# Optimization experiments

Measured on AMD Instinct MI355X. Metric: run time of the kernel, lower is better.

Reference implementation:

```python
import jax, jax.numpy as jnp
import numpy as np

N_NODES = 100000


def gcn_layer(x, W, b, src, dst, n):
    # PyG GCNConv: add self-loops, symmetric degree normalization,
    # message = norm * (x @ W)[src], aggregated (sum) at dst, plus bias.
    loops = jnp.arange(n, dtype=src.dtype)
    s = jnp.concatenate([src, loops])  # [E+N]
    d = jnp.concatenate([dst, loops])  # [E+N]
    deg = jnp.zeros((n,), x.dtype).at[d].add(jnp.ones((s.shape[0],), x.dtype))
    dinv = jnp.where(deg > 0, jax.lax.rsqrt(deg), 0.0)
    norm = dinv[s] * dinv[d]  # [E+N]
    h = x @ W  # [N, out]
    msg = h[s] * norm[:, None]  # [E+N, out]
    out = jax.ops.segment_sum(msg, d, num_segments=n)
    return out + b


def setup_inputs() -> dict:
    key = jax.random.key(0)
    k1, k2, k3, k4 = jax.random.split(key, 4)
    in_dim, hid_dim, out_dim = 128, 128, 64
    x = jax.random.normal(k1, (N_NODES, in_dim), dtype=jnp.float32)
    edge_index = jax.random.randint(k2, (2, 1600000), 0, N_NODES, dtype=jnp.int64)
    W1 = jax.random.normal(k3, (in_dim, hid_dim), dtype=jnp.float32) / np.sqrt(in_dim)
    b1 = jnp.zeros((hid_dim,), jnp.float32)
    W2 = jax.random.normal(k4, (hid_dim, out_dim), dtype=jnp.float32) / np.sqrt(hid_dim)
    b2 = jnp.zeros((out_dim,), jnp.float32)
    return {"x": x, "edge_index": edge_index, "W1": W1, "b1": b1, "W2": W2, "b2": b2}


def reference(x, edge_index, W1, b1, W2, b2):
    src, dst = edge_index[0], edge_index[1]
    h = gcn_layer(x, W1, b1, src, dst, N_NODES)
    h = jax.nn.relu(h)
    # F.dropout(training=False) -> identity (eval mode reference)
    out = gcn_layer(h, W2, b2, src, dst, N_NODES)
    return out
```

## Files before the change

kernel.cpp:

```cpp
#include <hip/hip_runtime.h>
#include <hip/hip_fp16.h>

#define NN 100000
#define NSB 256
#define WPS2 391
#define CAP2 8192
#define EPB 16

typedef _Float16 f16;
typedef _Float16 f16x8 __attribute__((ext_vector_type(8)));
typedef float f32x4 __attribute__((ext_vector_type(4)));

__device__ __forceinline__ int eload(const void* e, long i, int is64) {
  if (is64) return (int)((const long long*)e)[i];
  return ((const int*)e)[i];
}

__global__ __launch_bounds__(1024) void k_detect(const unsigned* __restrict__ e,
                                                 int* __restrict__ flag,
                                                 int* __restrict__ bcur2) {
  __shared__ unsigned red[1024];
  int t = threadIdx.x;
  if (t < NSB) bcur2[t] = t * CAP2;
  unsigned acc = e[1 + 2 * t] | e[1 + 2 * t + 2048];
  red[t] = acc;
  __syncthreads();
  for (int off = 512; off > 0; off >>= 1) {
    if (t < off) red[t] |= red[t + off];
    __syncthreads();
  }
  if (t == 0) *flag = (red[0] == 0) ? 1 : 0;
}

__global__ void k_wprep(const float* __restrict__ W1, const float* __restrict__ W2,
                        f16* __restrict__ Wt1, f16* __restrict__ Wt2) {
  int idx = blockIdx.x * 256 + threadIdx.x;
  if (idx < 128 * 128) {
    int k = idx / 128, n = idx % 128;
    Wt1[n * 128 + k] = (f16)W1[idx];
  } else {
    int i2 = idx - 128 * 128;
    if (i2 < 128 * 64) {
      int k = i2 / 64, n = i2 % 64;
      Wt2[n * 128 + k] = (f16)W2[i2];
    }
  }
}

__global__ __launch_bounds__(256) void k_split(const void* __restrict__ e,
                                               const int* __restrict__ flag,
                                               int E, int* __restrict__ bcur2,
                                               int* __restrict__ srcb,
                                               int* __restrict__ dstb) {
  __shared__ int hist[NSB];
  const int tid = threadIdx.x;
  const long b0 = (long)blockIdx.x * (256 * EPB);
  const int is64 = *flag;
  hist[tid] = 0;
  __syncthreads();

  int sv[EPB], dv[EPB];
#pragma unroll
  for (int j = 0; j < EPB; ++j) {
    long idx = b0 + j * 256 + tid;
    int s = 0, d = -1;
    if (idx < E) {
      s = eload(e, idx, is64);
      d = eload(e, (long)E + idx, is64);
    }
    sv[j] = s; dv[j] = d;
    if (d >= 0) atomicAdd(&hist[(unsigned)d / WPS2], 1);
  }
  __syncthreads();
  {
    int c = hist[tid];
    int base = (c > 0) ? atomicAdd(&bcur2[tid], c) : 0;
    __syncthreads();
    hist[tid] = base;
  }
  __syncthreads();
#pragma unroll
  for (int j = 0; j < EPB; ++j) {
    int d = dv[j];
    if (d < 0) continue;
    int pos = atomicAdd(&hist[(unsigned)d / WPS2], 1);
    srcb[pos] = sv[j];
    dstb[pos] = d;
  }
}

__global__ __launch_bounds__(256) void k_wscan(const int* __restrict__ bcur2,
                                               int* __restrict__ wbase,
                                               int* __restrict__ rowptr, int E) {
  __shared__ int sm[NSB];
  int t = threadIdx.x;
  int c = bcur2[t] - t * CAP2;
  sm[t] = c;
  __syncthreads();
  for (int off = 1; off < NSB; off <<= 1) {
    int a = (t >= off) ? sm[t - off] : 0;
    __syncthreads();
    sm[t] += a;
    __syncthreads();
  }
  wbase[t] = sm[t] - c;
  if (t == 0) rowptr[NN] = E;
}

__global__ __launch_bounds__(256) void k_build(const int* __restrict__ dstb,
                                               const int* __restrict__ srcb,
                                               const int* __restrict__ bcur2,
                                               const int* __restrict__ wbase,
                                               int* __restrict__ rowptr,
                                               float* __restrict__ dinv,
                                               int* __restrict__ csr) {
  __shared__ int lc[512];
  __shared__ int cur[512];
  const int tid = threadIdx.x;
  const int b = blockIdx.x;
  const int nlo = b * WPS2;
  const int nhi = (nlo + WPS2 < NN) ? nlo + WPS2 : NN;
  const int nw = nhi - nlo;
  lc[tid] = 0; lc[tid + 256] = 0;
  __syncthreads();
  const int cnt = bcur2[b] - b * CAP2;
  const long s0 = (long)b * CAP2;
  for (int i = tid; i < cnt; i += 256)
    atomicAdd(&lc[dstb[s0 + i] - nlo], 1);
  __syncthreads();
  for (int off = 1; off < 512; off <<= 1) {
    int a0 = (tid >= off) ? lc[tid - off] : 0;
    int a1 = (tid + 256 >= off) ? lc[tid + 256 - off] : 0;
    __syncthreads();
    lc[tid] += a0; lc[tid + 256] += a1;
    __syncthreads();
  }
  const int wb = wbase[b];
#pragma unroll
  for (int h = 0; h < 2; ++h) {
    int j = tid + h * 256;
    if (j < nw) {
      int inc = lc[j];
      int c = inc - (j > 0 ? lc[j - 1] : 0);
      int ex = wb + inc - c;
      rowptr[nlo + j] = ex;
      dinv[nlo + j] = rsqrtf((float)c + 1.0f);
      cur[j] = ex;
    }
  }
  __syncthreads();
  for (int i = tid; i < cnt; i += 256) {
    int d = dstb[s0 + i];
    int pos = atomicAdd(&cur[d - nlo], 1);
    csr[pos] = srcb[s0 + i];
  }
}

__global__ __launch_bounds__(256) void gemm_mfma(const float* __restrict__ X,
                                                 const f16* __restrict__ Wt,
                                                 const float* __restrict__ dinv,
                                                 f16* __restrict__ Y) {
  constexpr int NF = 8;
  __shared__ f16 Al[128 * 128];
  __shared__ f16 Bl[128 * 128];
  const int tid = threadIdx.x;
  const long row0 = (long)blockIdx.x * 128;

  for (int c = tid; c < 128 * 16; c += 256) {
    int n = c >> 4, g = c & 15;
    f16x8 v = *(const f16x8*)&Wt[n * 128 + g * 8];
    *(f16x8*)((char*)Bl + n * 256 + ((g * 16) ^ ((n & 7) << 4))) = v;
  }
  for (int c = tid; c < 2048; c += 256) {
    int r = c >> 4, g = c & 15;
    long grow = row0 + r;
    f16x8 v;
    if (grow < NN) {
      const float4* p = (const float4*)&X[grow * 128 + g * 8];
      float4 p0 = p[0], p1 = p[1];
      float f[8] = {p0.x, p0.y, p0.z, p0.w, p1.x, p1.y, p1.z, p1.w};
#pragma unroll
      for (int j = 0; j < 8; ++j) v[j] = (f16)f[j];
    } else {
#pragma unroll
      for (int j = 0; j < 8; ++j) v[j] = (f16)0;
    }
    *(f16x8*)((char*)Al + r * 256 + ((g * 16) ^ ((r & 7) << 4))) = v;
  }
  __syncthreads();

  const int l = tid & 63, w = tid >> 6;
  const int lm = l & 15, lg = l >> 4;
  const int r0 = w * 32 + lm, r1 = r0 + 16;

  f32x4 acc0[NF], acc1[NF];
#pragma unroll
  for (int nf = 0; nf < NF; ++nf) { acc0[nf] = (f32x4)(0.f); acc1[nf] = (f32x4)(0.f); }

#pragma unroll
  for (int kk = 0; kk < 4; ++kk) {
    const int kb = kk * 64 + lg * 16;
    f16x8 a0 = *(const f16x8*)((const char*)Al + r0 * 256 + (kb ^ ((r0 & 7) << 4)));
    f16x8 a1 = *(const f16x8*)((const char*)Al + r1 * 256 + (kb ^ ((r1 & 7) << 4)));
#pragma unroll
    for (int nf = 0; nf < NF; ++nf) {
      int n = nf * 16 + lm;
      f16x8 b = *(const f16x8*)((const char*)Bl + n * 256 + (kb ^ ((n & 7) << 4)));
      acc0[nf] = __builtin_amdgcn_mfma_f32_16x16x32_f16(a0, b, acc0[nf], 0, 0, 0);
      acc1[nf] = __builtin_amdgcn_mfma_f32_16x16x32_f16(a1, b, acc1[nf], 0, 0, 0);
    }
  }

#pragma unroll
  for (int reg = 0; reg < 4; ++reg) {
    long gr0 = row0 + w * 32 + lg * 4 + reg;
    long gr1 = gr0 + 16;
    float d0 = (gr0 < NN) ? dinv[gr0] : 0.f;
    float d1 = (gr1 < NN) ? dinv[gr1] : 0.f;
#pragma unroll
    for (int nf = 0; nf < NF; ++nf) {
      if (gr0 < NN) Y[gr0 * 128 + nf * 16 + lm] = (f16)(acc0[nf][reg] * d0);
      if (gr1 < NN) Y[gr1 * 128 + nf * 16 + lm] = (f16)(acc1[nf][reg] * d1);
    }
  }
}

__global__ __launch_bounds__(256) void k_aggemm(const f16* __restrict__ hn1,
                                                const int* __restrict__ rowptr,
                                                const int* __restrict__ csr,
                                                const float* __restrict__ dinv,
                                                const float* __restrict__ b1,
                                                const f16* __restrict__ Wt2,
                                                f16* __restrict__ hn2) {
  __shared__ f16 Al[64 * 128];
  __shared__ f16 Bl[64 * 128];
  const int tid = threadIdx.x;
  const long row0 = (long)blockIdx.x * 64;

  for (int c = tid; c < 64 * 16; c += 256) {
    int n = c >> 4, g = c & 15;
    f16x8 v = *(const f16x8*)&Wt2[n * 128 + g * 8];
    *(f16x8*)((char*)Bl + n * 256 + ((g * 16) ^ ((n & 7) << 4))) = v;
  }

  const int g = tid & 15;
  const int c8 = g * 8;
  const int rloc = tid >> 4;
  float4 bb0 = *(const float4*)&b1[c8];
  float4 bb1 = *(const float4*)&b1[c8 + 4];
  const float bb[8] = {bb0.x, bb0.y, bb0.z, bb0.w, bb1.x, bb1.y, bb1.z, bb1.w};

#pragma unroll
  for (int p = 0; p < 4; ++p) {
    int r = p * 16 + rloc;
    long dd = row0 + r;
    f16x8 v;
    if (dd < NN) {
      float acc[8];
      f16x8 sv = *(const f16x8*)&hn1[dd * 128 + c8];
#pragma unroll
      for (int j = 0; j < 8; ++j) acc[j] = (float)sv[j];
      int e = rowptr[dd];
      const int end = rowptr[dd + 1];
      for (; e + 4 <= end; e += 4) {
        int s0 = csr[e], s1 = csr[e + 1], s2 = csr[e + 2], s3 = csr[e + 3];
        f16x8 v0 = *(const f16x8*)&hn1[(long)s0 * 128 + c8];
        f16x8 v1 = *(const f16x8*)&hn1[(long)s1 * 128 + c8];
        f16x8 v2 = *(const f16x8*)&hn1[(long)s2 * 128 + c8];
        f16x8 v3 = *(const f16x8*)&hn1[(long)s3 * 128 + c8];
#pragma unroll
        for (int j = 0; j < 8; ++j)
          acc[j] += ((float)v0[j] + (float)v1[j]) + ((float)v2[j] + (float)v3[j]);
      }
      for (; e < end; ++e) {
        int s = csr[e];
        f16x8 v0 = *(const f16x8*)&hn1[(long)s * 128 + c8];
#pragma unroll
        for (int j = 0; j < 8; ++j) acc[j] += (float)v0[j];
      }
      float ddv = dinv[dd];
#pragma unroll
      for (int j = 0; j < 8; ++j) {
        float t = fmaxf(acc[j] * ddv + bb[j], 0.f);
        v[j] = (f16)t;
      }
    } else {
#pragma unroll
      for (int j = 0; j < 8; ++j) v[j] = (f16)0;
    }
    *(f16x8*)((char*)Al + r * 256 + ((g * 16) ^ ((r & 7) << 4))) = v;
  }
  __syncthreads();

  const int l = tid & 63, w = tid >> 6;
  const int lm = l & 15, lg = l >> 4;
  const int r0 = w * 16 + lm;

  f32x4 acc0[4];
#pragma unroll
  for (int nf = 0; nf < 4; ++nf) acc0[nf] = (f32x4)(0.f);

#pragma unroll
  for (int kk = 0; kk < 4; ++kk) {
    const int kb = kk * 64 + lg * 16;
    f16x8 a0 = *(const f16x8*)((const char*)Al + r0 * 256 + (kb ^ ((r0 & 7) << 4)));
#pragma unroll
    for (int nf = 0; nf < 4; ++nf) {
      int n = nf * 16 + lm;
      f16x8 b = *(const f16x8*)((const char*)Bl + n * 256 + (kb ^ ((n & 7) << 4)));
      acc0[nf] = __builtin_amdgcn_mfma_f32_16x16x32_f16(a0, b, acc0[nf], 0, 0, 0);
    }
  }

#pragma unroll
  for (int reg = 0; reg < 4; ++reg) {
    long gr0 = row0 + w * 16 + lg * 4 + reg;
    if (gr0 < NN) {
      float d0 = dinv[gr0];
#pragma unroll
      for (int nf = 0; nf < 4; ++nf)
        hn2[gr0 * 64 + nf * 16 + lm] = (f16)(acc0[nf][reg] * d0);
    }
  }
}

__global__ __launch_bounds__(256) void k_agg2(const __half* __restrict__ hn,
                                              const int* __restrict__ rowptr,
                                              const int* __restrict__ csr,
                                              const float* __restrict__ dinv,
                                              const float* __restrict__ bias,
                                              float* __restrict__ out) {
  constexpr int C = 64, TP = 8;
  long t = (long)blockIdx.x * 256 + threadIdx.x;
  int d = (int)(t / TP);
  if (d >= NN) return;
  int c8 = (int)(t % TP) * 8;

  float acc[8];
  {
    float4 raw = *(const float4*)&hn[(long)d * C + c8];
    const __half2* h2 = (const __half2*)&raw;
#pragma unroll
    for (int q = 0; q < 4; ++q) {
      float2 f = __half22float2(h2[q]);
      acc[2 * q] = f.x; acc[2 * q + 1] = f.y;
    }
  }
  int e = rowptr[d];
  const int end = rowptr[d + 1];

  for (; e + 8 <= end; e += 8) {
    float4 r[8];
#pragma unroll
    for (int u = 0; u < 8; ++u) r[u] = *(const float4*)&hn[(long)csr[e + u] * C + c8];
#pragma unroll
    for (int u = 0; u < 8; ++u) {
      const __half2* a0 = (const __half2*)&r[u];
#pragma unroll
      for (int q = 0; q < 4; ++q) {
        float2 f0 = __half22float2(a0[q]);
        acc[2 * q] += f0.x; acc[2 * q + 1] += f0.y;
      }
    }
  }
  for (; e + 4 <= end; e += 4) {
    float4 r[4];
#pragma unroll
    for (int u = 0; u < 4; ++u) r[u] = *(const float4*)&hn[(long)csr[e + u] * C + c8];
#pragma unroll
    for (int u = 0; u < 4; ++u) {
      const __half2* a0 = (const __half2*)&r[u];
#pragma unroll
      for (int q = 0; q < 4; ++q) {
        float2 f0 = __half22float2(a0[q]);
        acc[2 * q] += f0.x; acc[2 * q + 1] += f0.y;
      }
    }
  }
  for (; e < end; ++e) {
    float4 r0 = *(const float4*)&hn[(long)csr[e] * C + c8];
    const __half2* a0 = (const __half2*)&r0;
#pragma unroll
    for (int q = 0; q < 4; ++q) {
      float2 f0 = __half22float2(a0[q]);
      acc[2 * q] += f0.x; acc[2 * q + 1] += f0.y;
    }
  }

  float dd = dinv[d];
  float4 b0 = *(const float4*)&bias[c8];
  float4 b1 = *(const float4*)&bias[c8 + 4];
  *(float4*)&out[(long)d * C + c8] =
      make_float4(acc[0] * dd + b0.x, acc[1] * dd + b0.y,
                  acc[2] * dd + b0.z, acc[3] * dd + b0.w);
  *(float4*)&out[(long)d * C + c8 + 4] =
      make_float4(acc[4] * dd + b1.x, acc[5] * dd + b1.y,
                  acc[6] * dd + b1.z, acc[7] * dd + b1.w);
}

extern "C" void kernel_launch(void* const* d_in, const int* in_sizes, int n_in,
                              void* d_out, int out_size, void* d_ws, size_t ws_size,
                              hipStream_t stream) {
  const float* x  = (const float*)d_in[0];
  const void*  ep = d_in[1];
  const float* W1 = (const float*)d_in[2];
  const float* b1 = (const float*)d_in[3];
  const float* W2 = (const float*)d_in[4];
  const float* b2 = (const float*)d_in[5];
  float* out = (float*)d_out;
  const int E = in_sizes[1] / 2;

  float*  wsf    = (float*)d_ws;
  int*    wsi    = (int*)d_ws;
  int*    flag   = wsi;
  int*    bcur2  = wsi + 64;
  int*    wbase  = wsi + 320;
  float*  dinv   = wsf + 576;
  int*    rowptr = wsi + 100576;
  f16*    Wt1    = (f16*)(wsi + 200640);
  f16*    Wt2    = (f16*)(wsi + 208832);
  int*    csr    = wsi + 212992;
  int*    srcb   = wsi + 1812992;
  int*    dstb   = wsi + 3910144;
  f16*    hn1    = (f16*)(wsi + 6007296);
  f16*    hn2    = (f16*)(wsi + 12407296);

  const int SB = (E + 256 * EPB - 1) / (256 * EPB);
  const int GB = (NN + 127) / 128;
  const int FB = (NN + 63) / 64;

  k_detect<<<1, 1024, 0, stream>>>((const unsigned*)ep, flag, bcur2);
  k_wprep<<<96, 256, 0, stream>>>(W1, W2, Wt1, Wt2);
  k_split<<<SB, 256, 0, stream>>>(ep, flag, E, bcur2, srcb, dstb);
  k_wscan<<<1, 256, 0, stream>>>(bcur2, wbase, rowptr, E);
  k_build<<<NSB, 256, 0, stream>>>(dstb, srcb, bcur2, wbase, rowptr, dinv, csr);

  gemm_mfma<<<GB, 256, 0, stream>>>(x, Wt1, dinv, hn1);
  k_aggemm<<<FB, 256, 0, stream>>>(hn1, rowptr, csr, dinv, b1, Wt2, hn2);
  k_agg2<<<(NN * 8 + 255) / 256, 256, 0, stream>>>(
      (const __half*)hn2, rowptr, csr, dinv, b2, out);
}
```

Before: 193.5 us.

## Unfuse layer-1 aggregation from layer-2 GEMM and share a templated interleaved aggregator

Splits the fused aggregate-then-GEMM kernel into a standalone aggregation kernel that writes the ReLU-free layer-1 activations to an fp16 buffer, followed by a templated MFMA GEMM that applies ReLU on load. Both aggregation passes now use one templated kernel in which each thread processes two destination nodes interleaved, to raise memory-level parallelism in the gather. This adds an extra global round trip of the hidden activations in exchange for better occupancy and less LDS pressure in the gather phase.

```diff
diff --git a/kernel.cpp b/kernel.cpp
--- a/kernel.cpp
+++ b/kernel.cpp
@@ -156,17 +156,18 @@
   }
 }
 
-__global__ __launch_bounds__(256) void gemm_mfma(const float* __restrict__ X,
+template <int COUT, bool RELU, typename TIN>
+__global__ __launch_bounds__(256) void gemm_mfma(const TIN* __restrict__ X,
                                                  const f16* __restrict__ Wt,
                                                  const float* __restrict__ dinv,
                                                  f16* __restrict__ Y) {
-  constexpr int NF = 8;
+  constexpr int NF = COUT / 16;
   __shared__ f16 Al[128 * 128];
-  __shared__ f16 Bl[128 * 128];
+  __shared__ f16 Bl[COUT * 128];
   const int tid = threadIdx.x;
   const long row0 = (long)blockIdx.x * 128;
 
-  for (int c = tid; c < 128 * 16; c += 256) {
+  for (int c = tid; c < COUT * 16; c += 256) {
     int n = c >> 4, g = c & 15;
     f16x8 v = *(const f16x8*)&Wt[n * 128 + g * 8];
     *(f16x8*)((char*)Bl + n * 256 + ((g * 16) ^ ((n & 7) << 4))) = v;
@@ -176,11 +177,22 @@
     long grow = row0 + r;
     f16x8 v;
     if (grow < NN) {
-      const float4* p = (const float4*)&X[grow * 128 + g * 8];
-      float4 p0 = p[0], p1 = p[1];
-      float f[8] = {p0.x, p0.y, p0.z, p0.w, p1.x, p1.y, p1.z, p1.w};
-#pragma unroll
-      for (int j = 0; j < 8; ++j) v[j] = (f16)f[j];
+      if constexpr (sizeof(TIN) == 4) {
+        const float4* p = (const float4*)&X[grow * 128 + g * 8];
+        float4 p0 = p[0], p1 = p[1];
+        float f[8] = {p0.x, p0.y, p0.z, p0.w, p1.x, p1.y, p1.z, p1.w};
+#pragma unroll
+        for (int j = 0; j < 8; ++j) {
+          float t = RELU ? fmaxf(f[j], 0.f) : f[j];
+          v[j] = (f16)t;
+        }
+      } else {
+        v = *(const f16x8*)&X[grow * 128 + g * 8];
+        if (RELU) {
+#pragma unroll
+          for (int j = 0; j < 8; ++j) v[j] = v[j] > (f16)0 ? v[j] : (f16)0;
+        }
+      }
     } else {
 #pragma unroll
       for (int j = 0; j < 8; ++j) v[j] = (f16)0;
@@ -219,183 +231,106 @@
     float d1 = (gr1 < NN) ? dinv[gr1] : 0.f;
 #pragma unroll
     for (int nf = 0; nf < NF; ++nf) {
-      if (gr0 < NN) Y[gr0 * 128 + nf * 16 + lm] = (f16)(acc0[nf][reg] * d0);
-      if (gr1 < NN) Y[gr1 * 128 + nf * 16 + lm] = (f16)(acc1[nf][reg] * d1);
-    }
-  }
-}
-
-__global__ __launch_bounds__(256) void k_aggemm(const f16* __restrict__ hn1,
-                                                const int* __restrict__ rowptr,
-                                                const int* __restrict__ csr,
-                                                const float* __restrict__ dinv,
-                                                const float* __restrict__ b1,
-                                                const f16* __restrict__ Wt2,
-                                                f16* __restrict__ hn2) {
-  __shared__ f16 Al[64 * 128];
-  __shared__ f16 Bl[64 * 128];
+      if (gr0 < NN) Y[gr0 * COUT + nf * 16 + lm] = (f16)(acc0[nf][reg] * d0);
+      if (gr1 < NN) Y[gr1 * COUT + nf * 16 + lm] = (f16)(acc1[nf][reg] * d1);
+    }
+  }
+}
+
+__device__ __forceinline__ void acc8f(float* acc, const __half* p) {
+  float4 raw = *(const float4*)p;
+  const __half2* h = (const __half2*)&raw;
+#pragma unroll
+  for (int q = 0; q < 4; ++q) {
+    float2 f = __half22float2(h[q]);
+    acc[2 * q] += f.x; acc[2 * q + 1] += f.y;
+  }
+}
+
+template <int C, typename TOUT>
+__global__ __launch_bounds__(256) void k_agg_i(const __half* __restrict__ hn,
+                                               const int* __restrict__ rowptr,
+                                               const int* __restrict__ csr,
+                                               const float* __restrict__ dinv,
+                                               const float* __restrict__ bias,
+                                               TOUT* __restrict__ out) {
+  constexpr int TP = C / 8;
+  constexpr int SLOTS = 256 / TP;
   const int tid = threadIdx.x;
-  const long row0 = (long)blockIdx.x * 64;
-
-  for (int c = tid; c < 64 * 16; c += 256) {
-    int n = c >> 4, g = c & 15;
-    f16x8 v = *(const f16x8*)&Wt2[n * 128 + g * 8];
-    *(f16x8*)((char*)Bl + n * 256 + ((g * 16) ^ ((n & 7) << 4))) = v;
-  }
-
-  const int g = tid & 15;
-  const int c8 = g * 8;
-  const int rloc = tid >> 4;
-  float4 bb0 = *(const float4*)&b1[c8];
-  float4 bb1 = *(const float4*)&b1[c8 + 4];
-  const float bb[8] = {bb0.x, bb0.y, bb0.z, bb0.w, bb1.x, bb1.y, bb1.z, bb1.w};
-
-#pragma unroll
-  for (int p = 0; p < 4; ++p) {
-    int r = p * 16 + rloc;
-    long dd = row0 + r;
-    f16x8 v;
-    if (dd < NN) {
-      float acc[8];
-      f16x8 sv = *(const f16x8*)&hn1[dd * 128 + c8];
-#pragma unroll
-      for (int j = 0; j < 8; ++j) acc[j] = (float)sv[j];
-      int e = rowptr[dd];
-      const int end = rowptr[dd + 1];
-      for (; e + 4 <= end; e += 4) {
-        int s0 = csr[e], s1 = csr[e + 1], s2 = csr[e + 2], s3 = csr[e + 3];
-        f16x8 v0 = *(const f16x8*)&hn1[(long)s0 * 128 + c8];
-        f16x8 v1 = *(const f16x8*)&hn1[(long)s1 * 128 + c8];
-        f16x8 v2 = *(const f16x8*)&hn1[(long)s2 * 128 + c8];
-        f16x8 v3 = *(const f16x8*)&hn1[(long)s3 * 128 + c8];
-#pragma unroll
-        for (int j = 0; j < 8; ++j)
-          acc[j] += ((float)v0[j] + (float)v1[j]) + ((float)v2[j] + (float)v3[j]);
-      }
-      for (; e < end; ++e) {
-        int s = csr[e];
-        f16x8 v0 = *(const f16x8*)&hn1[(long)s * 128 + c8];
-#pragma unroll
-        for (int j = 0; j < 8; ++j) acc[j] += (float)v0[j];
-      }
-      float ddv = dinv[dd];
-#pragma unroll
-      for (int j = 0; j < 8; ++j) {
-        float t = fmaxf(acc[j] * ddv + bb[j], 0.f);
-        v[j] = (f16)t;
-      }
+  const int slot = tid / TP;
+  const int c8 = (tid % TP) * 8;
+  const long dA = (long)blockIdx.x * (2 * SLOTS) + slot;
+  const long dB = dA + SLOTS;
+
+  float accA[8] = {0, 0, 0, 0, 0, 0, 0, 0};
+  float accB[8] = {0, 0, 0, 0, 0, 0, 0, 0};
+  int eA = 0, endA = 0, eB = 0, endB = 0;
+  if (dA < NN) {
+    eA = rowptr[dA]; endA = rowptr[dA + 1];
+    acc8f(accA, &hn[dA * C + c8]);
+  }
+  if (dB < NN) {
+    eB = rowptr[dB]; endB = rowptr[dB + 1];
+    acc8f(accB, &hn[dB * C + c8]);
+  }
+
+  int nA = endA - eA, nB = endB - eB;
+  int both = (nA < nB ? nA : nB) >> 2;
+  for (int it = 0; it < both; ++it) {
+    int a0 = csr[eA], a1 = csr[eA + 1], a2 = csr[eA + 2], a3 = csr[eA + 3];
+    int b0 = csr[eB], b1 = csr[eB + 1], b2 = csr[eB + 2], b3 = csr[eB + 3];
+    acc8f(accA, &hn[(long)a0 * C + c8]);
+    acc8f(accB, &hn[(long)b0 * C + c8]);
+    acc8f(accA, &hn[(long)a1 * C + c8]);
+    acc8f(accB, &hn[(long)b1 * C + c8]);
+    acc8f(accA, &hn[(long)a2 * C + c8]);
+    acc8f(accB, &hn[(long)b2 * C + c8]);
+    acc8f(accA, &hn[(long)a3 * C + c8]);
+    acc8f(accB, &hn[(long)b3 * C + c8]);
+    eA += 4; eB += 4;
+  }
+  for (; eA + 4 <= endA; eA += 4) {
+    int a0 = csr[eA], a1 = csr[eA + 1], a2 = csr[eA + 2], a3 = csr[eA + 3];
+    acc8f(accA, &hn[(long)a0 * C + c8]);
+    acc8f(accA, &hn[(long)a1 * C + c8]);
+    acc8f(accA, &hn[(long)a2 * C + c8]);
+    acc8f(accA, &hn[(long)a3 * C + c8]);
+  }
+  for (; eA < endA; ++eA) acc8f(accA, &hn[(long)csr[eA] * C + c8]);
+  for (; eB + 4 <= endB; eB += 4) {
+    int b0 = csr[eB], b1 = csr[eB + 1], b2 = csr[eB + 2], b3 = csr[eB + 3];
+    acc8f(accB, &hn[(long)b0 * C + c8]);
+    acc8f(accB, &hn[(long)b1 * C + c8]);
+    acc8f(accB, &hn[(long)b2 * C + c8]);
+    acc8f(accB, &hn[(long)b3 * C + c8]);
+  }
+  for (; eB < endB; ++eB) acc8f(accB, &hn[(long)csr[eB] * C + c8]);
+
+  float4 bv0 = *(const float4*)&bias[c8];
+  float4 bv1 = *(const float4*)&bias[c8 + 4];
+  const float bb[8] = {bv0.x, bv0.y, bv0.z, bv0.w, bv1.x, bv1.y, bv1.z, bv1.w};
+
+#pragma unroll
+  for (int h = 0; h < 2; ++h) {
+    long d = h ? dB : dA;
+    if (d >= NN) continue;
+    float* acc = h ? accB : accA;
+    float dd = dinv[d];
+    float o[8];
+#pragma unroll
+    for (int j = 0; j < 8; ++j) o[j] = acc[j] * dd + bb[j];
+    if constexpr (sizeof(TOUT) == 2) {
+      __half2 hp[4];
+      hp[0] = __floats2half2_rn(o[0], o[1]);
+      hp[1] = __floats2half2_rn(o[2], o[3]);
+      hp[2] = __floats2half2_rn(o[4], o[5]);
+      hp[3] = __floats2half2_rn(o[6], o[7]);
+      *(float4*)&out[d * C + c8] = *(float4*)hp;
     } else {
-#pragma unroll
-      for (int j = 0; j < 8; ++j) v[j] = (f16)0;
-    }
-    *(f16x8*)((char*)Al + r * 256 + ((g * 16) ^ ((r & 7) << 4))) = v;
-  }
-  __syncthreads();
-
-  const int l = tid & 63, w = tid >> 6;
-  const int lm = l & 15, lg = l >> 4;
-  const int r0 = w * 16 + lm;
-
-  f32x4 acc0[4];
-#pragma unroll
-  for (int nf = 0; nf < 4; ++nf) acc0[nf] = (f32x4)(0.f);
-
-#pragma unroll
-  for (int kk = 0; kk < 4; ++kk) {
-    const int kb = kk * 64 + lg * 16;
-    f16x8 a0 = *(const f16x8*)((const char*)Al + r0 * 256 + (kb ^ ((r0 & 7) << 4)));
-#pragma unroll
-    for (int nf = 0; nf < 4; ++nf) {
-      int n = nf * 16 + lm;
-      f16x8 b = *(const f16x8*)((const char*)Bl + n * 256 + (kb ^ ((n & 7) << 4)));
-      acc0[nf] = __builtin_amdgcn_mfma_f32_16x16x32_f16(a0, b, acc0[nf], 0, 0, 0);
-    }
-  }
-
-#pragma unroll
-  for (int reg = 0; reg < 4; ++reg) {
-    long gr0 = row0 + w * 16 + lg * 4 + reg;
-    if (gr0 < NN) {
-      float d0 = dinv[gr0];
-#pragma unroll
-      for (int nf = 0; nf < 4; ++nf)
-        hn2[gr0 * 64 + nf * 16 + lm] = (f16)(acc0[nf][reg] * d0);
-    }
-  }
-}
-
-__global__ __launch_bounds__(256) void k_agg2(const __half* __restrict__ hn,
-                                              const int* __restrict__ rowptr,
-                                              const int* __restrict__ csr,
-                                              const float* __restrict__ dinv,
-                                              const float* __restrict__ bias,
-                                              float* __restrict__ out) {
-  constexpr int C = 64, TP = 8;
-  long t = (long)blockIdx.x * 256 + threadIdx.x;
-  int d = (int)(t / TP);
-  if (d >= NN) return;
-  int c8 = (int)(t % TP) * 8;
-
-  float acc[8];
-  {
-    float4 raw = *(const float4*)&hn[(long)d * C + c8];
-    const __half2* h2 = (const __half2*)&raw;
-#pragma unroll
-    for (int q = 0; q < 4; ++q) {
-      float2 f = __half22float2(h2[q]);
-      acc[2 * q] = f.x; acc[2 * q + 1] = f.y;
-    }
-  }
-  int e = rowptr[d];
-  const int end = rowptr[d + 1];
-
-  for (; e + 8 <= end; e += 8) {
-    float4 r[8];
-#pragma unroll
-    for (int u = 0; u < 8; ++u) r[u] = *(const float4*)&hn[(long)csr[e + u] * C + c8];
-#pragma unroll
-    for (int u = 0; u < 8; ++u) {
-      const __half2* a0 = (const __half2*)&r[u];
-#pragma unroll
-      for (int q = 0; q < 4; ++q) {
-        float2 f0 = __half22float2(a0[q]);
-        acc[2 * q] += f0.x; acc[2 * q + 1] += f0.y;
-      }
-    }
-  }
-  for (; e + 4 <= end; e += 4) {
-    float4 r[4];
-#pragma unroll
-    for (int u = 0; u < 4; ++u) r[u] = *(const float4*)&hn[(long)csr[e + u] * C + c8];
-#pragma unroll
-    for (int u = 0; u < 4; ++u) {
-      const __half2* a0 = (const __half2*)&r[u];
-#pragma unroll
-      for (int q = 0; q < 4; ++q) {
-        float2 f0 = __half22float2(a0[q]);
-        acc[2 * q] += f0.x; acc[2 * q + 1] += f0.y;
-      }
-    }
-  }
-  for (; e < end; ++e) {
-    float4 r0 = *(const float4*)&hn[(long)csr[e] * C + c8];
-    const __half2* a0 = (const __half2*)&r0;
-#pragma unroll
-    for (int q = 0; q < 4; ++q) {
-      float2 f0 = __half22float2(a0[q]);
-      acc[2 * q] += f0.x; acc[2 * q + 1] += f0.y;
-    }
-  }
-
-  float dd = dinv[d];
-  float4 b0 = *(const float4*)&bias[c8];
-  float4 b1 = *(const float4*)&bias[c8 + 4];
-  *(float4*)&out[(long)d * C + c8] =
-      make_float4(acc[0] * dd + b0.x, acc[1] * dd + b0.y,
-                  acc[2] * dd + b0.z, acc[3] * dd + b0.w);
-  *(float4*)&out[(long)d * C + c8 + 4] =
-      make_float4(acc[4] * dd + b1.x, acc[5] * dd + b1.y,
-                  acc[6] * dd + b1.z, acc[7] * dd + b1.w);
+      *(float4*)&out[d * C + c8]     = make_float4(o[0], o[1], o[2], o[3]);
+      *(float4*)&out[d * C + c8 + 4] = make_float4(o[4], o[5], o[6], o[7]);
+    }
+  }
 }
 
 extern "C" void kernel_launch(void* const* d_in, const int* in_sizes, int n_in,
@@ -423,11 +358,13 @@
   int*    srcb   = wsi + 1812992;
   int*    dstb   = wsi + 3910144;
   f16*    hn1    = (f16*)(wsi + 6007296);
-  f16*    hn2    = (f16*)(wsi + 12407296);
+  f16*    a1     = (f16*)(wsi + 12407296);
+  f16*    hn2    = hn1;
 
   const int SB = (E + 256 * EPB - 1) / (256 * EPB);
   const int GB = (NN + 127) / 128;
-  const int FB = (NN + 63) / 64;
+  const int AB1 = (NN + 31) / 32;
+  const int AB2 = (NN + 63) / 64;
 
   k_detect<<<1, 1024, 0, stream>>>((const unsigned*)ep, flag, bcur2);
   k_wprep<<<96, 256, 0, stream>>>(W1, W2, Wt1, Wt2);
@@ -435,8 +372,11 @@
   k_wscan<<<1, 256, 0, stream>>>(bcur2, wbase, rowptr, E);
   k_build<<<NSB, 256, 0, stream>>>(dstb, srcb, bcur2, wbase, rowptr, dinv, csr);
 
-  gemm_mfma<<<GB, 256, 0, stream>>>(x, Wt1, dinv, hn1);
-  k_aggemm<<<FB, 256, 0, stream>>>(hn1, rowptr, csr, dinv, b1, Wt2, hn2);
-  k_agg2<<<(NN * 8 + 255) / 256, 256, 0, stream>>>(
+  gemm_mfma<128, false, float><<<GB, 256, 0, stream>>>(x, Wt1, dinv, hn1);
+  k_agg_i<128, __half><<<AB1, 256, 0, stream>>>(
+      (const __half*)hn1, rowptr, csr, dinv, b1, (__half*)a1);
+
+  gemm_mfma<64, true, f16><<<GB, 256, 0, stream>>>(a1, Wt2, dinv, hn2);
+  k_agg_i<64, float><<<AB2, 256, 0, stream>>>(
       (const __half*)hn2, rowptr, csr, dinv, b2, out);
 }
```

New measurement: 212.8 us. 1.1x slower.
